# Optimization experiments

Hardware: AMD Instinct MI355X
Metric: run time of the kernel (lower is better)

Reference implementation:

```python
import jax, jax.numpy as jnp
import numpy as np

B, S, D, N, H = 4, 1024, 768, 12, 64
IGNORE = -100000.0


def setup_inputs() -> dict:
    key = jax.random.key(0)
    ks = jax.random.split(key, 9)
    std = 0.02
    return {
        "normalized_resid_pre": jax.random.normal(ks[0], (B, S, D), dtype=jnp.float32),
        "W_Q": jax.random.normal(ks[1], (N, D, H), dtype=jnp.float32) * std,
        "W_K": jax.random.normal(ks[2], (N, D, H), dtype=jnp.float32) * std,
        "W_V": jax.random.normal(ks[3], (N, D, H), dtype=jnp.float32) * std,
        "W_O": jax.random.normal(ks[4], (N, H, D), dtype=jnp.float32) * std,
        "b_Q": jnp.zeros((N, H), dtype=jnp.float32),
        "b_K": jnp.zeros((N, H), dtype=jnp.float32),
        "b_V": jnp.zeros((N, H), dtype=jnp.float32),
        "b_O": jnp.zeros((D,), dtype=jnp.float32),
    }


def reference(normalized_resid_pre, W_Q, W_K, W_V, W_O, b_Q, b_K, b_V, b_O):
    x = normalized_resid_pre  # [b, s, d]
    d_head = W_Q.shape[-1]
    # per-head projections: [b, n, s, h]
    Q = jnp.einsum("bsd,ndh->bnsh", x, W_Q) + b_Q[None, :, None, :]
    K = jnp.einsum("bsd,ndh->bnsh", x, W_K) + b_K[None, :, None, :]
    V = jnp.einsum("bsd,ndh->bnsh", x, W_V) + b_V[None, :, None, :]
    # scores [b, n, s_q, s_k]
    scores = jnp.einsum("bnqh,bnkh->bnqk", Q, K) / jnp.sqrt(jnp.float32(d_head))
    s = scores.shape[-1]
    # original: tril(scores) + triu(IGNORE, k=1) == where(causal, scores, IGNORE)
    causal = jnp.tril(jnp.ones((s, s), dtype=bool))
    masked = jnp.where(causal[None, None], scores, jnp.float32(IGNORE))
    probs = jax.nn.softmax(masked, axis=-1)
    # z [b, s_q, n, h]
    z = jnp.einsum("bnqk,bnkh->bqnh", probs, V)
    out = jnp.einsum("bqnh,nhd->bqd", z, W_O) + b_O
    return out
```

## Files before the change

kernel.cpp:

```cpp
#include <hip/hip_runtime.h>

typedef __bf16 bf16x8 __attribute__((ext_vector_type(8)));
typedef __bf16 bf16x4 __attribute__((ext_vector_type(4)));
typedef float  f32x4  __attribute__((ext_vector_type(4)));
typedef float  f32x16 __attribute__((ext_vector_type(16)));

constexpr int B_ = 4, S_ = 1024, D_ = 768, N_ = 12, H_ = 64;
constexpr int BNSH = B_ * N_ * S_ * H_;
constexpr float SCALE2 = 0.18033688011f;

__device__ __forceinline__ f32x4 mfma16(bf16x8 a, bf16x8 b, f32x4 c) {
    return __builtin_amdgcn_mfma_f32_16x16x32_bf16(a, b, c, 0, 0, 0);
}
__device__ __forceinline__ f32x16 mfma32(bf16x8 a, bf16x8 b, f32x16 c) {
    return __builtin_amdgcn_mfma_f32_32x32x16_bf16(a, b, c, 0, 0, 0);
}

__device__ __forceinline__ unsigned pkbf16(float a, float b) {
    unsigned r;
    asm("v_cvt_pk_bf16_f32 %0, %1, %2" : "=v"(r) : "v"(a), "v"(b));
    return r;
}

__device__ __forceinline__ void gload16(const __bf16* g, __bf16* l) {
    __builtin_amdgcn_global_load_lds(
        (const __attribute__((address_space(1))) unsigned int*)g,
        (__attribute__((address_space(3))) unsigned int*)l, 16, 0, 0);
}

__device__ __forceinline__ void stage128x64(const __bf16* g, int ld, __bf16* lds,
                                            int wid, int lane) {
    #pragma unroll
    for (int i = 0; i < 4; ++i) {
        int cb = (wid * 4 + i) * 64;
        int chunk = cb + lane;
        int r = chunk >> 3, p = chunk & 7;
        int q = p ^ (r & 7);
        gload16(g + (size_t)r * ld + q * 8, lds + cb * 8);
    }
}
__device__ __forceinline__ void stage64x64(const __bf16* g, int ld, __bf16* lds,
                                           int wid, int lane) {
    #pragma unroll
    for (int i = 0; i < 2; ++i) {
        int cb = (wid * 2 + i) * 64;
        int chunk = cb + lane;
        int r = chunk >> 3, p = chunk & 7;
        int q = p ^ (r & 7);
        gload16(g + (size_t)r * ld + q * 8, lds + cb * 8);
    }
}
__device__ __forceinline__ void stage64x64_w2(const __bf16* g, int ld, __bf16* lds,
                                              int wid, int lane) {
    #pragma unroll
    for (int i = 0; i < 4; ++i) {
        int cb = (wid * 4 + i) * 64;
        int chunk = cb + lane;
        int r = chunk >> 3, p = chunk & 7;
        int q = p ^ (r & 7);
        gload16(g + (size_t)r * ld + q * 8, lds + cb * 8);
    }
}

__global__ __launch_bounds__(256) void prep_kernel(
    const float* __restrict__ x,
    const float* __restrict__ wq, const float* __restrict__ wk,
    const float* __restrict__ wv, const float* __restrict__ wo,
    __bf16* __restrict__ xb, __bf16* __restrict__ wt, __bf16* __restrict__ wot) {
    __shared__ __bf16 T[64][65];
    const int blk = blockIdx.x;
    const int tid = threadIdx.x;
    if (blk < 768) {
        int base = blk * 1024 + tid;
        #pragma unroll
        for (int i = 0; i < 4; ++i) {
            int idx = base + i * 256;
            float4 v = ((const float4*)x)[idx];
            bf16x4 o;
            o[0] = (__bf16)v.x; o[1] = (__bf16)v.y;
            o[2] = (__bf16)v.z; o[3] = (__bf16)v.w;
            ((bf16x4*)xb)[idx] = o;
        }
        return;
    }
    int rr = tid >> 4, c4 = (tid & 15) * 4;
    if (blk < 1200) {
        int t = blk - 768;
        int dt = t % 12, mh = t / 12;
        int mat = mh / 12, n = mh % 12;
        const float* in = (mat == 0 ? wq : mat == 1 ? wk : wv) + (size_t)n * 768 * 64;
        __bf16* outp = wt + (size_t)(mat * 768 + n * 64) * 768;
        int d0 = dt * 64;
        #pragma unroll
        for (int i = 0; i < 4; ++i) {
            int row = rr + 16 * i;
            float4 v = *(const float4*)&in[(size_t)(d0 + row) * 64 + c4];
            T[c4 + 0][row] = (__bf16)v.x;
            T[c4 + 1][row] = (__bf16)v.y;
            T[c4 + 2][row] = (__bf16)v.z;
            T[c4 + 3][row] = (__bf16)v.w;
        }
        __syncthreads();
        #pragma unroll
        for (int i = 0; i < 4; ++i) {
            int hrow = rr + 16 * i;
            bf16x4 o;
            o[0] = T[hrow][c4 + 0]; o[1] = T[hrow][c4 + 1];
            o[2] = T[hrow][c4 + 2]; o[3] = T[hrow][c4 + 3];
            *(bf16x4*)&outp[(size_t)hrow * 768 + d0 + c4] = o;
        }
    } else {
        int t = blk - 1200;
        int r0 = (t % 12) * 64, c0 = (t / 12) * 64;
        #pragma unroll
        for (int i = 0; i < 4; ++i) {
            int row = rr + 16 * i;
            float4 v = *(const float4*)&wo[(size_t)(r0 + row) * 768 + c0 + c4];
            T[c4 + 0][row] = (__bf16)v.x;
            T[c4 + 1][row] = (__bf16)v.y;
            T[c4 + 2][row] = (__bf16)v.z;
            T[c4 + 3][row] = (__bf16)v.w;
        }
        __syncthreads();
        #pragma unroll
        for (int i = 0; i < 4; ++i) {
            int crow = rr + 16 * i;
            bf16x4 o;
            o[0] = T[crow][c4 + 0]; o[1] = T[crow][c4 + 1];
            o[2] = T[crow][c4 + 2]; o[3] = T[crow][c4 + 3];
            *(bf16x4*)&wot[(size_t)(c0 + crow) * 768 + r0 + c4] = o;
        }
    }
}

__global__ __launch_bounds__(256) void qkv_gemm(
    const __bf16* __restrict__ xb, const __bf16* __restrict__ wtg,
    const float* __restrict__ bq, const float* __restrict__ bk,
    const float* __restrict__ bv,
    __bf16* __restrict__ Qb, __bf16* __restrict__ Kb, __bf16* __restrict__ Vtb) {
    __shared__ __bf16 As[2][128 * 64];
    __shared__ __bf16 Bs[2][64 * 64];
    const int m0 = blockIdx.x * 128;
    const int j0 = blockIdx.y * 64;
    const int tid = threadIdx.x, wid = tid >> 6, lane = tid & 63;
    const int quad = lane >> 4, lrow = lane & 15;
    const int l3 = lrow & 7;
    int koff[2];
    #pragma unroll
    for (int ks = 0; ks < 2; ++ks)
        koff[ks] = lrow * 64 + ((ks * 4 + quad) ^ l3) * 8;

    f32x4 zf = {0.f, 0.f, 0.f, 0.f};
    f32x4 acc[2][4];
    #pragma unroll
    for (int i = 0; i < 2; ++i)
        #pragma unroll
        for (int j = 0; j < 4; ++j) acc[i][j] = zf;

    stage128x64(xb + (size_t)m0 * 768, 768, As[0], wid, lane);
    stage64x64(wtg + (size_t)j0 * 768, 768, Bs[0], wid, lane);

    for (int kt = 0; kt < 12; ++kt) {
        const int buf = kt & 1;
        __syncthreads();
        if (kt < 11) {
            stage128x64(xb + (size_t)m0 * 768 + (kt + 1) * 64, 768, As[buf ^ 1], wid, lane);
            stage64x64(wtg + (size_t)j0 * 768 + (kt + 1) * 64, 768, Bs[buf ^ 1], wid, lane);
        }
        #pragma unroll
        for (int ks = 0; ks < 2; ++ks) {
            bf16x8 af[2], bfr[4];
            #pragma unroll
            for (int mi = 0; mi < 2; ++mi)
                af[mi] = *(const bf16x8*)(As[buf] + (wid * 32 + mi * 16) * 64 + koff[ks]);
            #pragma unroll
            for (int ni = 0; ni < 4; ++ni)
                bfr[ni] = *(const bf16x8*)(Bs[buf] + ni * 1024 + koff[ks]);
            #pragma unroll
            for (int mi = 0; mi < 2; ++mi)
                #pragma unroll
                for (int ni = 0; ni < 4; ++ni)
                    acc[mi][ni] = mfma16(af[mi], bfr[ni], acc[mi][ni]);
        }
    }

    const int mat = j0 / 768;
    const int n = (j0 % 768) >> 6;
    const int b = m0 >> 10;
    const int s_base = (m0 & 1023) + wid * 32;
    const float* bias = (mat == 0 ? bq : mat == 1 ? bk : bv) + n * 64;
    const float osc = (mat == 0) ? SCALE2 : 1.0f;
    float bias_v[4];
    #pragma unroll
    for (int ni = 0; ni < 4; ++ni) bias_v[ni] = bias[ni * 16 + lrow];

    if (mat == 2) {
        __bf16* vout = Vtb + (size_t)(b * N_ + n) * 64 * 1024;
        #pragma unroll
        for (int mi = 0; mi < 2; ++mi)
            #pragma unroll
            for (int ni = 0; ni < 4; ++ni) {
                int h = ni * 16 + lrow;
                int s0 = s_base + mi * 16 + quad * 4;
                bf16x4 pv;
                #pragma unroll
                for (int r = 0; r < 4; ++r)
                    pv[r] = (__bf16)(acc[mi][ni][r] + bias_v[ni]);
                *(bf16x4*)(vout + (size_t)h * 1024 + s0) = pv;
            }
    } else {
        __bf16* qk = (mat == 0 ? Qb : Kb) + (size_t)(b * N_ + n) * 1024 * 64;
        #pragma unroll
        for (int mi = 0; mi < 2; ++mi)
            #pragma unroll
            for (int r = 0; r < 4; ++r) {
                int s = s_base + mi * 16 + quad * 4 + r;
                #pragma unroll
                for (int ni = 0; ni < 4; ++ni)
                    qk[(size_t)s * 64 + ni * 16 + lrow] =
                        (__bf16)((acc[mi][ni][r] + bias_v[ni]) * osc);
            }
    }
}

__global__ __launch_bounds__(128) void attn_mfma(
    const __bf16* __restrict__ Qb, const __bf16* __restrict__ Kb,
    const __bf16* __restrict__ Vtb, __bf16* __restrict__ zb) {
    __shared__ __bf16 Ks[2][64 * 64], Vs[2][64 * 64];
    const int bid = blockIdx.x;
    const int qt = 15 - bid / 48;
    const int bn = bid % 48;
    const int b = bn / N_, n = bn % N_;
    const int tid = threadIdx.x, wid = tid >> 6, lane = tid & 63;
    const int col = lane & 31;
    const int hi  = lane >> 5;
    const int c7  = col & 7;
    const __bf16* Qg = Qb + (size_t)(b * N_ + n) * S_ * H_;
    const __bf16* Kg = Kb + (size_t)(b * N_ + n) * S_ * H_;
    const __bf16* Vg = Vtb + (size_t)(b * N_ + n) * H_ * S_;
    const int q0 = qt * 64;
    const int qloc = wid * 32 + col;

    bf16x8 qf[4];
    #pragma unroll
    for (int kk = 0; kk < 4; ++kk)
        qf[kk] = *(const bf16x8*)&Qg[(size_t)(q0 + qloc) * 64 + kk * 16 + hi * 8];

    int rowb[2];
    #pragma unroll
    for (int i = 0; i < 2; ++i) rowb[i] = (i * 32 + col) * 64;

    stage64x64_w2(Kg, 64, Ks[0], wid, lane);
    stage64x64_w2(Vg, 1024, Vs[0], wid, lane);

    const f32x16 zf16 = {0.f,0.f,0.f,0.f,0.f,0.f,0.f,0.f,
                         0.f,0.f,0.f,0.f,0.f,0.f,0.f,0.f};
    f32x16 o[2];
    o[0] = zf16; o[1] = zf16;
    float l_r = 0.f;

    auto do_tile = [&](int buf, bool diag) {
        f32x16 sc[2];
        sc[0] = zf16; sc[1] = zf16;
        __builtin_amdgcn_s_setprio(1);
        #pragma unroll
        for (int sb = 0; sb < 2; ++sb)
            #pragma unroll
            for (int kk = 0; kk < 4; ++kk) {
                bf16x8 kf = *(const bf16x8*)(Ks[buf] + rowb[sb]
                                             + ((kk * 2 + hi) ^ c7) * 8);
                sc[sb] = mfma32(kf, qf[kk], sc[sb]);
            }
        __builtin_amdgcn_s_setprio(0);
        if (diag) {
            #pragma unroll
            for (int sb = 0; sb < 2; ++sb)
                #pragma unroll
                for (int r = 0; r < 16; ++r) {
                    int sl = sb * 32 + (r & 3) + 8 * (r >> 2) + 4 * hi;
                    if (sl > qloc) sc[sb][r] = -1e30f;
                }
        }
        float rs = 0.f;
        #pragma unroll
        for (int sb = 0; sb < 2; ++sb)
            #pragma unroll
            for (int r = 0; r < 16; ++r) {
                float p = __builtin_amdgcn_exp2f(sc[sb][r]);
                sc[sb][r] = p;
                rs += p;
            }
        l_r += rs;
        bf16x8 pf[4];
        #pragma unroll
        for (int kk = 0; kk < 4; ++kk) {
            const int sb = kk >> 1, base = (kk & 1) * 8;
            unsigned A0 = pkbf16(sc[sb][base + 0], sc[sb][base + 1]);
            unsigned A1 = pkbf16(sc[sb][base + 2], sc[sb][base + 3]);
            unsigned B0 = pkbf16(sc[sb][base + 4], sc[sb][base + 5]);
            unsigned B1 = pkbf16(sc[sb][base + 6], sc[sb][base + 7]);
            asm volatile("v_permlane32_swap_b32 %0, %1" : "+v"(A0), "+v"(B0));
            asm volatile("v_permlane32_swap_b32 %0, %1" : "+v"(A1), "+v"(B1));
            union { unsigned w[4]; bf16x8 v; } u;
            u.w[0] = A0; u.w[1] = A1; u.w[2] = B0; u.w[3] = B1;
            pf[kk] = u.v;
        }
        __builtin_amdgcn_s_setprio(1);
        #pragma unroll
        for (int hb = 0; hb < 2; ++hb)
            #pragma unroll
            for (int kk = 0; kk < 4; ++kk) {
                bf16x8 vf = *(const bf16x8*)(Vs[buf] + rowb[hb]
                                             + ((kk * 2 + hi) ^ c7) * 8);
                o[hb] = mfma32(vf, pf[kk], o[hb]);
            }
        __builtin_amdgcn_s_setprio(0);
    };

    for (int kt = 0; kt < qt; ++kt) {
        __syncthreads();
        stage64x64_w2(Kg + (size_t)(kt + 1) * 64 * 64, 64, Ks[(kt + 1) & 1], wid, lane);
        stage64x64_w2(Vg + (kt + 1) * 64, 1024, Vs[(kt + 1) & 1], wid, lane);
        do_tile(kt & 1, false);
    }
    __syncthreads();
    do_tile(qt & 1, true);

    float lt = l_r + __shfl_xor(l_r, 32);
    const float linv = 1.0f / lt;
    __bf16* zout = zb + (size_t)b * S_ * 768 + (size_t)(q0 + qloc) * 768 + n * 64;
    #pragma unroll
    for (int hb = 0; hb < 2; ++hb)
        #pragma unroll
        for (int rq = 0; rq < 4; ++rq) {
            bf16x4 zo;
            #pragma unroll
            for (int j = 0; j < 4; ++j)
                zo[j] = (__bf16)(o[hb][rq * 4 + j] * linv);
            *(bf16x4*)&zout[hb * 32 + rq * 8 + hi * 4] = zo;
        }
}

__global__ __launch_bounds__(256) void out_gemm(
    const __bf16* __restrict__ zb, const __bf16* __restrict__ wot,
    const float* __restrict__ bo, float* __restrict__ out) {
    __shared__ __bf16 As[2][64 * 64];
    __shared__ __bf16 Bs[2][64 * 64];
    const int m0 = blockIdx.x * 64;
    const int j0 = blockIdx.y * 64;
    const int tid = threadIdx.x, wid = tid >> 6, lane = tid & 63;
    const int quad = lane >> 4, lrow = lane & 15;
    const int l3 = lrow & 7;
    int koff[2];
    #pragma unroll
    for (int ks = 0; ks < 2; ++ks)
        koff[ks] = lrow * 64 + ((ks * 4 + quad) ^ l3) * 8;

    f32x4 zf = {0.f, 0.f, 0.f, 0.f};
    f32x4 acc[4];
    #pragma unroll
    for (int j = 0; j < 4; ++j) acc[j] = zf;

    stage64x64(zb + (size_t)m0 * 768, 768, As[0], wid, lane);
    stage64x64(wot + (size_t)j0 * 768, 768, Bs[0], wid, lane);

    for (int kt = 0; kt < 12; ++kt) {
        const int buf = kt & 1;
        __syncthreads();
        if (kt < 11) {
            stage64x64(zb + (size_t)m0 * 768 + (kt + 1) * 64, 768, As[buf ^ 1], wid, lane);
            stage64x64(wot + (size_t)j0 * 768 + (kt + 1) * 64, 768, Bs[buf ^ 1], wid, lane);
        }
        #pragma unroll
        for (int ks = 0; ks < 2; ++ks) {
            bf16x8 af = *(const bf16x8*)(As[buf] + wid * 1024 + koff[ks]);
            #pragma unroll
            for (int ni = 0; ni < 4; ++ni) {
                bf16x8 bfr = *(const bf16x8*)(Bs[buf] + ni * 1024 + koff[ks]);
                acc[ni] = mfma16(af, bfr, acc[ni]);
            }
        }
    }

    float bias_v[4];
    #pragma unroll
    for (int ni = 0; ni < 4; ++ni) bias_v[ni] = bo[j0 + ni * 16 + lrow];
    #pragma unroll
    for (int r = 0; r < 4; ++r) {
        int m = m0 + wid * 16 + quad * 4 + r;
        #pragma unroll
        for (int ni = 0; ni < 4; ++ni)
            out[(size_t)m * 768 + j0 + ni * 16 + lrow] = acc[ni][r] + bias_v[ni];
    }
}

extern "C" void kernel_launch(void* const* d_in, const int* in_sizes, int n_in,
                              void* d_out, int out_size, void* d_ws, size_t ws_size,
                              hipStream_t stream) {
    const float* x  = (const float*)d_in[0];
    const float* wq = (const float*)d_in[1];
    const float* wk = (const float*)d_in[2];
    const float* wv = (const float*)d_in[3];
    const float* wo = (const float*)d_in[4];
    const float* bq = (const float*)d_in[5];
    const float* bk = (const float*)d_in[6];
    const float* bv = (const float*)d_in[7];
    const float* bo = (const float*)d_in[8];
    float* out = (float*)d_out;

    __bf16* p   = (__bf16*)d_ws;
    __bf16* xb  = p;  p += (size_t)4096 * 768;
    __bf16* wt  = p;  p += (size_t)2304 * 768;
    __bf16* wot = p;  p += (size_t)768 * 768;
    __bf16* Qb  = p;  p += (size_t)BNSH;
    __bf16* Kb  = p;  p += (size_t)BNSH;
    __bf16* Vtb = p;  p += (size_t)BNSH;
    __bf16* zb  = p;  p += (size_t)4096 * 768;

    prep_kernel<<<1344, 256, 0, stream>>>(x, wq, wk, wv, wo, xb, wt, wot);
    qkv_gemm<<<dim3(32, 36), 256, 0, stream>>>(xb, wt, bq, bk, bv, Qb, Kb, Vtb);
    attn_mfma<<<768, 128, 0, stream>>>(Qb, Kb, Vtb, zb);
    out_gemm<<<dim3(64, 12), 256, 0, stream>>>(zb, wot, bo, out);
}
```

Measured before the change: 141.2 us.

## Split attention KV tiles across two wave groups and merge partials via LDS

The attention kernel goes from 128 to 256 threads. Two wave pairs take alternating KV tiles, with staging spread across all four waves. At the end the second group writes its partial O accumulators and row sums to shared memory, and the first group adds them, normalizes and stores z. The aim is more waves in flight to hide latency and halve per-wave staging work. The cost is the extra LDS and merge step, and each wave group sits idle at the per-iteration barrier while the other computes.

Result: no change. 140.1 us (-0.8%).

```diff
diff --git a/kernel.cpp b/kernel.cpp
--- a/kernel.cpp
+++ b/kernel.cpp
@@ -44,17 +44,6 @@
     #pragma unroll
     for (int i = 0; i < 2; ++i) {
         int cb = (wid * 2 + i) * 64;
-        int chunk = cb + lane;
-        int r = chunk >> 3, p = chunk & 7;
-        int q = p ^ (r & 7);
-        gload16(g + (size_t)r * ld + q * 8, lds + cb * 8);
-    }
-}
-__device__ __forceinline__ void stage64x64_w2(const __bf16* g, int ld, __bf16* lds,
-                                              int wid, int lane) {
-    #pragma unroll
-    for (int i = 0; i < 4; ++i) {
-        int cb = (wid * 4 + i) * 64;
         int chunk = cb + lane;
         int r = chunk >> 3, p = chunk & 7;
         int q = p ^ (r & 7);
@@ -223,15 +212,18 @@
     }
 }
 
-__global__ __launch_bounds__(128) void attn_mfma(
+__global__ __launch_bounds__(256) void attn_mfma(
     const __bf16* __restrict__ Qb, const __bf16* __restrict__ Kb,
     const __bf16* __restrict__ Vtb, __bf16* __restrict__ zb) {
     __shared__ __bf16 Ks[2][64 * 64], Vs[2][64 * 64];
+    __shared__ float MS[2][64][33];
     const int bid = blockIdx.x;
     const int qt = 15 - bid / 48;
     const int bn = bid % 48;
     const int b = bn / N_, n = bn % N_;
     const int tid = threadIdx.x, wid = tid >> 6, lane = tid & 63;
+    const int wq = wid & 1;
+    const int wk = wid >> 1;
     const int col = lane & 31;
     const int hi  = lane >> 5;
     const int c7  = col & 7;
@@ -239,7 +231,7 @@
     const __bf16* Kg = Kb + (size_t)(b * N_ + n) * S_ * H_;
     const __bf16* Vg = Vtb + (size_t)(b * N_ + n) * H_ * S_;
     const int q0 = qt * 64;
-    const int qloc = wid * 32 + col;
+    const int qloc = wq * 32 + col;
 
     bf16x8 qf[4];
     #pragma unroll
@@ -250,8 +242,8 @@
     #pragma unroll
     for (int i = 0; i < 2; ++i) rowb[i] = (i * 32 + col) * 64;
 
-    stage64x64_w2(Kg, 64, Ks[0], wid, lane);
-    stage64x64_w2(Vg, 1024, Vs[0], wid, lane);
+    stage64x64(Kg, 64, Ks[0], wid, lane);
+    stage64x64(Vg, 1024, Vs[0], wid, lane);
 
     const f32x16 zf16 = {0.f,0.f,0.f,0.f,0.f,0.f,0.f,0.f,
                          0.f,0.f,0.f,0.f,0.f,0.f,0.f,0.f};
@@ -317,28 +309,47 @@
         __builtin_amdgcn_s_setprio(0);
     };
 
-    for (int kt = 0; kt < qt; ++kt) {
+    const int nt = qt + 1;
+    for (int kt = 0; kt < nt; ++kt) {
         __syncthreads();
-        stage64x64_w2(Kg + (size_t)(kt + 1) * 64 * 64, 64, Ks[(kt + 1) & 1], wid, lane);
-        stage64x64_w2(Vg + (kt + 1) * 64, 1024, Vs[(kt + 1) & 1], wid, lane);
-        do_tile(kt & 1, false);
-    }
+        if (kt + 1 < nt) {
+            stage64x64(Kg + (size_t)(kt + 1) * 64 * 64, 64, Ks[(kt + 1) & 1], wid, lane);
+            stage64x64(Vg + (kt + 1) * 64, 1024, Vs[(kt + 1) & 1], wid, lane);
+        }
+        if ((kt & 1) == wk) do_tile(kt & 1, kt == qt);
+    }
+
     __syncthreads();
-    do_tile(qt & 1, true);
-
-    float lt = l_r + __shfl_xor(l_r, 32);
-    const float linv = 1.0f / lt;
-    __bf16* zout = zb + (size_t)b * S_ * 768 + (size_t)(q0 + qloc) * 768 + n * 64;
-    #pragma unroll
-    for (int hb = 0; hb < 2; ++hb)
-        #pragma unroll
-        for (int rq = 0; rq < 4; ++rq) {
-            bf16x4 zo;
-            #pragma unroll
-            for (int j = 0; j < 4; ++j)
-                zo[j] = (__bf16)(o[hb][rq * 4 + j] * linv);
-            *(bf16x4*)&zout[hb * 32 + rq * 8 + hi * 4] = zo;
-        }
+    if (wk) {
+        #pragma unroll
+        for (int hb = 0; hb < 2; ++hb)
+            #pragma unroll
+            for (int r = 0; r < 16; ++r)
+                MS[wq][lane][hb * 16 + r] = o[hb][r];
+        MS[wq][lane][32] = l_r;
+    }
+    __syncthreads();
+    if (!wk) {
+        #pragma unroll
+        for (int hb = 0; hb < 2; ++hb)
+            #pragma unroll
+            for (int r = 0; r < 16; ++r)
+                o[hb][r] += MS[wq][lane][hb * 16 + r];
+        l_r += MS[wq][lane][32];
+        float lt = l_r + __shfl_xor(l_r, 32);
+        const float linv = 1.0f / lt;
+        __bf16* zout = zb + (size_t)b * S_ * 768 + (size_t)(q0 + qloc) * 768 + n * 64;
+        #pragma unroll
+        for (int hb = 0; hb < 2; ++hb)
+            #pragma unroll
+            for (int rq = 0; rq < 4; ++rq) {
+                bf16x4 zo;
+                #pragma unroll
+                for (int j = 0; j < 4; ++j)
+                    zo[j] = (__bf16)(o[hb][rq * 4 + j] * linv);
+                *(bf16x4*)&zout[hb * 32 + rq * 8 + hi * 4] = zo;
+            }
+    }
 }
 
 __global__ __launch_bounds__(256) void out_gemm(
@@ -419,6 +430,6 @@
 
     prep_kernel<<<1344, 256, 0, stream>>>(x, wq, wk, wv, wo, xb, wt, wot);
     qkv_gemm<<<dim3(32, 36), 256, 0, stream>>>(xb, wt, bq, bk, bv, Qb, Kb, Vtb);
-    attn_mfma<<<768, 128, 0, stream>>>(Qb, Kb, Vtb, zb);
+    attn_mfma<<<768, 256, 0, stream>>>(Qb, Kb, Vtb, zb);
     out_gemm<<<dim3(64, 12), 256, 0, stream>>>(zb, wot, bo, out);
 }
```
